# Kernel tuning notes

Measured on AMD Instinct MI355X. Metric: run time of the kernel, lower is better.

## Reference

```python
import jax, jax.numpy as jnp
import numpy as np

B, PATCH_NUM, EMBED, DEC_EMBED, IN_CHANS, PSIZE3, NPTS = 32, 196, 768, 512, 6, 4096, 100000


def setup_inputs() -> dict:
    key = jax.random.key(0)
    ks = jax.random.split(key, 12)
    s = 0.02
    return {
        "sel_features": jax.random.normal(ks[0], (NPTS, IN_CHANS), jnp.float32),
        "coords_rela_query": jax.random.randint(ks[1], (NPTS,), 0, PSIZE3),
        "patch_unq_inv": jax.random.randint(ks[2], (NPTS,), 0, B * PATCH_NUM),
        "pad_idx": jnp.arange(B * PATCH_NUM),
        "coords_abs_cut": jax.random.normal(ks[3], (B * PATCH_NUM, 3), jnp.float32),
        "sel_coors": jax.random.normal(ks[4], (NPTS, 3), jnp.float32),
        "batch_size": B,
        "proj_weights": jnp.ones((PSIZE3, IN_CHANS, EMBED), jnp.float32),
        "w1_enc": jax.random.normal(ks[5], (3, EMBED), jnp.float32) * s,
        "b1_enc": jnp.zeros((EMBED,), jnp.float32),
        "w2_enc": jax.random.normal(ks[6], (EMBED, EMBED), jnp.float32) * s,
        "b2_enc": jnp.zeros((EMBED,), jnp.float32),
        "w1_dec": jax.random.normal(ks[7], (3, DEC_EMBED), jnp.float32) * s,
        "b1_dec": jnp.zeros((DEC_EMBED,), jnp.float32),
        "w2_dec": jax.random.normal(ks[8], (DEC_EMBED, DEC_EMBED), jnp.float32) * s,
        "b2_dec": jnp.zeros((DEC_EMBED,), jnp.float32),
    }


def _mlp(x, w1, b1, w2, b2):
    # nn.Linear -> GELU (exact erf, torch default) -> nn.Linear
    h = jax.nn.gelu(x @ w1 + b1, approximate=False)
    return h @ w2 + b2


def reference(sel_features, coords_rela_query, patch_unq_inv, pad_idx,
              coords_abs_cut, sel_coors, batch_size, proj_weights,
              w1_enc, b1_enc, w2_enc, b2_enc, w1_dec, b1_dec, w2_dec, b2_dec):
    num_seg = batch_size * PATCH_NUM
    feats = jnp.einsum('nc,ncd->nd', sel_features, proj_weights[coords_rela_query])  # [N_pts, D]
    # scatter-mean over patch segment ids
    seg_sum = jax.ops.segment_sum(feats, patch_unq_inv, num_segments=num_seg)
    cnt = jax.ops.segment_sum(jnp.ones((feats.shape[0],), feats.dtype), patch_unq_inv, num_segments=num_seg)
    seg_mean = seg_sum / jnp.maximum(cnt, 1.0)[:, None]
    # masked scatter into padded [B*patch_num, D] tensor
    features_patch = jnp.zeros((num_seg, EMBED), feats.dtype).at[pad_idx].set(seg_mean)
    features_patch = features_patch.reshape(batch_size, PATCH_NUM, EMBED)
    coords = coords_abs_cut.reshape(batch_size, PATCH_NUM, 3)
    pos_emb_enc = _mlp(coords, w1_enc, b1_enc, w2_enc, b2_enc)
    pos_emb_dec = _mlp(coords, w1_dec, b1_dec, w2_dec, b2_dec)
    # sel_features is returned detached in the original
    return (features_patch + pos_emb_enc,
            jax.lax.stop_gradient(sel_features),
            sel_coors,
            pos_emb_dec)
```

## Files before the change

### kernel.cpp

```cpp
#include <hip/hip_runtime.h>
#include <hip/hip_bf16.h>
#include <cmath>

#define NTHREADS 256

constexpr int IN_CHANS = 6;
constexpr int EMBED = 768;
constexpr int DEC_EMBED = 512;

typedef __attribute__((ext_vector_type(8))) short short8;
typedef __attribute__((ext_vector_type(4))) float f32x4;

__device__ __forceinline__ void gload_lds16(const short* g, short* l) {
    __builtin_amdgcn_global_load_lds((const __attribute__((address_space(1))) void*)g,
                                     (__attribute__((address_space(3))) void*)l, 16, 0, 0);
}

__device__ __forceinline__ float gelu_f(float x) {
    return 0.5f * x * (1.0f + erff(x * 0.70710678118654752f));
}


__global__ void zero_kernel(int* __restrict__ p, int n) {
    int i = blockIdx.x * blockDim.x + threadIdx.x;
    if (i < n) p[i] = 0;
}


__global__ void hc_kernel(const float* __restrict__ coords,
                          const float* __restrict__ w1e, const float* __restrict__ b1e,
                          const float* __restrict__ w1d, const float* __restrict__ b1d,
                          const int* __restrict__ seg, const int* __restrict__ pad_idx,
                          const float* __restrict__ sel, const float* __restrict__ selc,
                          const float* __restrict__ w2e, const float* __restrict__ w2d,
                          __hip_bfloat16* __restrict__ hE, __hip_bfloat16* __restrict__ hD,
                          __hip_bfloat16* __restrict__ w2tE, __hip_bfloat16* __restrict__ w2tD,
                          int* __restrict__ segcnt, float* __restrict__ segsum,
                          int* __restrict__ inv,
                          float* __restrict__ out1, float* __restrict__ out2,
                          int hcBlocks, int num_seg, int npts) {
    __shared__ float tile[32][33];
    int bid = blockIdx.x;
    if (bid >= hcBlocks) {
        int b = bid - hcBlocks;
        const float* src; __hip_bfloat16* dst; int n;
        const int ntE = (EMBED / 32) * (EMBED / 32);
        if (b < ntE) { src = w2e; dst = w2tE; n = EMBED; }
        else         { b -= ntE; src = w2d; dst = w2tD; n = DEC_EMBED; }
        int tpr = n / 32;
        int tr = b / tpr, tc = b % tpr;
        int tx = threadIdx.x & 31, ty = threadIdx.x >> 5;
        #pragma unroll
        for (int i = 0; i < 4; ++i)
            tile[ty + 8 * i][tx] = src[(size_t)(tr * 32 + ty + 8 * i) * n + tc * 32 + tx];
        __syncthreads();
        #pragma unroll
        for (int i = 0; i < 4; ++i)
            dst[(size_t)(tc * 32 + ty + 8 * i) * n + tr * 32 + tx] =
                __float2bfloat16(tile[tx][ty + 8 * i]);
        return;
    }
    const unsigned nE8 = (unsigned)num_seg * (EMBED / 8);
    const unsigned nD8 = (unsigned)num_seg * (DEC_EMBED / 8);
    const unsigned t0 = nE8;
    const unsigned t1 = t0 + nD8;
    const unsigned t2 = t1 + (unsigned)npts;
    const unsigned t2b = t2 + (unsigned)num_seg;
    const unsigned n14 = (unsigned)npts * IN_CHANS / 4;
    const unsigned t3 = t2b + n14;
    const unsigned n24 = (unsigned)npts * 3 / 4;
    const unsigned t4 = t3 + n24;
    const unsigned stride = (unsigned)hcBlocks * blockDim.x;
    for (unsigned idx = bid * blockDim.x + threadIdx.x; idx < t4; idx += stride) {
        if (idx < t0) {
            unsigned r = idx / (EMBED / 8), d = (idx % (EMBED / 8)) * 8;
            float c0 = coords[r * 3 + 0], c1 = coords[r * 3 + 1], c2 = coords[r * 3 + 2];
            float4 wa0 = *reinterpret_cast<const float4*>(w1e + 0 * EMBED + d);
            float4 wa1 = *reinterpret_cast<const float4*>(w1e + 0 * EMBED + d + 4);
            float4 wb0 = *reinterpret_cast<const float4*>(w1e + 1 * EMBED + d);
            float4 wb1 = *reinterpret_cast<const float4*>(w1e + 1 * EMBED + d + 4);
            float4 wc0 = *reinterpret_cast<const float4*>(w1e + 2 * EMBED + d);
            float4 wc1 = *reinterpret_cast<const float4*>(w1e + 2 * EMBED + d + 4);
            float4 bb0 = *reinterpret_cast<const float4*>(b1e + d);
            float4 bb1 = *reinterpret_cast<const float4*>(b1e + d + 4);
            union { short8 v; __hip_bfloat16 h[8]; } u;
            #pragma unroll
            for (int i = 0; i < 4; ++i)
                u.h[i] = __float2bfloat16(gelu_f(c0 * (&wa0.x)[i] + c1 * (&wb0.x)[i]
                                               + c2 * (&wc0.x)[i] + (&bb0.x)[i]));
            #pragma unroll
            for (int i = 0; i < 4; ++i)
                u.h[4 + i] = __float2bfloat16(gelu_f(c0 * (&wa1.x)[i] + c1 * (&wb1.x)[i]
                                                   + c2 * (&wc1.x)[i] + (&bb1.x)[i]));
            *reinterpret_cast<short8*>(&hE[(size_t)r * EMBED + d]) = u.v;
        } else if (idx < t1) {
            unsigned j = idx - t0;
            unsigned r = j / (DEC_EMBED / 8), d = (j % (DEC_EMBED / 8)) * 8;
            float c0 = coords[r * 3 + 0], c1 = coords[r * 3 + 1], c2 = coords[r * 3 + 2];
            float4 wa0 = *reinterpret_cast<const float4*>(w1d + 0 * DEC_EMBED + d);
            float4 wa1 = *reinterpret_cast<const float4*>(w1d + 0 * DEC_EMBED + d + 4);
            float4 wb0 = *reinterpret_cast<const float4*>(w1d + 1 * DEC_EMBED + d);
            float4 wb1 = *reinterpret_cast<const float4*>(w1d + 1 * DEC_EMBED + d + 4);
            float4 wc0 = *reinterpret_cast<const float4*>(w1d + 2 * DEC_EMBED + d);
            float4 wc1 = *reinterpret_cast<const float4*>(w1d + 2 * DEC_EMBED + d + 4);
            float4 bb0 = *reinterpret_cast<const float4*>(b1d + d);
            float4 bb1 = *reinterpret_cast<const float4*>(b1d + d + 4);
            union { short8 v; __hip_bfloat16 h[8]; } u;
            #pragma unroll
            for (int i = 0; i < 4; ++i)
                u.h[i] = __float2bfloat16(gelu_f(c0 * (&wa0.x)[i] + c1 * (&wb0.x)[i]
                                               + c2 * (&wc0.x)[i] + (&bb0.x)[i]));
            #pragma unroll
            for (int i = 0; i < 4; ++i)
                u.h[4 + i] = __float2bfloat16(gelu_f(c0 * (&wa1.x)[i] + c1 * (&wb1.x)[i]
                                                   + c2 * (&wc1.x)[i] + (&bb1.x)[i]));
            *reinterpret_cast<short8*>(&hD[(size_t)r * DEC_EMBED + d]) = u.v;
        } else if (idx < t2) {
            int i = (int)(idx - t1);
            int s = seg[i];
            atomicAdd(&segcnt[s], 1);
            const float2* s2 = reinterpret_cast<const float2*>(sel + (size_t)i * IN_CHANS);
            float2 a = s2[0], b = s2[1], c = s2[2];
            unsafeAtomicAdd(&segsum[s], a.x + a.y + b.x + b.y + c.x + c.y);
        } else if (idx < t2b) {
            int s = (int)(idx - t2);
            inv[pad_idx[s]] = s;
        } else if (idx < t3) {
            unsigned j = idx - t2b;
            reinterpret_cast<float4*>(out1)[j] =
                reinterpret_cast<const float4*>(sel)[j];
        } else {
            unsigned j = idx - t3;
            reinterpret_cast<float4*>(out2)[j] =
                reinterpret_cast<const float4*>(selc)[j];
        }
    }
}


__global__ void fallback_fix_kernel(const int* __restrict__ notones,
                                    const float* __restrict__ sel,
                                    const int* __restrict__ q,
                                    const int* __restrict__ seg,
                                    const int* __restrict__ segcnt,
                                    const float* __restrict__ segsum,
                                    const int* __restrict__ pad_idx,
                                    const float* __restrict__ W,
                                    float* __restrict__ out0, int npts, int num_seg) {
    if (*notones == 0) return;
    long totalP = (long)npts * (EMBED / 4);
    long totalS = (long)num_seg * (EMBED / 4);
    long total = totalP + totalS;
    for (long idx = blockIdx.x * (long)blockDim.x + threadIdx.x; idx < total;
         idx += (long)gridDim.x * blockDim.x) {
        if (idx < totalP) {
            int n = (int)(idx / (EMBED / 4));
            int d4 = (int)(idx % (EMBED / 4)) * 4;
            int s = seg[n];
            float invc = 1.0f / (float)max(segcnt[s], 1);
            const float* Wr = W + (size_t)q[n] * IN_CHANS * EMBED + d4;
            float acc[4] = {0.f, 0.f, 0.f, 0.f};
            #pragma unroll
            for (int c = 0; c < IN_CHANS; ++c) {
                float sv = sel[(size_t)n * IN_CHANS + c];
                float4 wv = *reinterpret_cast<const float4*>(Wr + c * EMBED);
                acc[0] += sv * wv.x; acc[1] += sv * wv.y;
                acc[2] += sv * wv.z; acc[3] += sv * wv.w;
            }
            size_t j = (size_t)pad_idx[s];
            #pragma unroll
            for (int i = 0; i < 4; ++i)
                unsafeAtomicAdd(&out0[j * EMBED + d4 + i], acc[i] * invc);
        } else {
            long j2 = idx - totalP;
            int s = (int)(j2 / (EMBED / 4));
            int d4 = (int)(j2 % (EMBED / 4)) * 4;
            float mean = segsum[s] / (float)max(segcnt[s], 1);
            size_t j = (size_t)pad_idx[s];
            #pragma unroll
            for (int i = 0; i < 4; ++i)
                unsafeAtomicAdd(&out0[j * EMBED + d4 + i], -mean);
        }
    }
}


__global__ __launch_bounds__(256, 6)
void gemm_lds_kernel(const __hip_bfloat16* __restrict__ hE,
                     const __hip_bfloat16* __restrict__ w2tE,
                     const float* __restrict__ b2e,
                     const __hip_bfloat16* __restrict__ hD,
                     const __hip_bfloat16* __restrict__ w2tD,
                     const float* __restrict__ b2d,
                     const float* __restrict__ Wproj,
                     const float* __restrict__ segsum,
                     const int* __restrict__ segcnt,
                     const int* __restrict__ inv,
                     int* __restrict__ notones,
                     float* __restrict__ out0, float* __restrict__ out3,
                     int M, int nblkE, int nblkTot, int ckBlocks, int psize3) {
    int bid = blockIdx.x;
    if (bid < ckBlocks) {
        const unsigned total4 = (unsigned)psize3 * (IN_CHANS * EMBED / 4);
        const unsigned stride4 = (unsigned)ckBlocks * blockDim.x * 4u;
        const float4* p = reinterpret_cast<const float4*>(Wproj);
        bool bad = false;
        for (unsigned i = ((unsigned)bid * blockDim.x + threadIdx.x) * 4u; i < total4;
             i += stride4) {
            float4 v0 = p[i], v1 = p[i + 1], v2 = p[i + 2], v3 = p[i + 3];
            bad |= v0.x != 1.f || v0.y != 1.f || v0.z != 1.f || v0.w != 1.f;
            bad |= v1.x != 1.f || v1.y != 1.f || v1.z != 1.f || v1.w != 1.f;
            bad |= v2.x != 1.f || v2.y != 1.f || v2.z != 1.f || v2.w != 1.f;
            bad |= v3.x != 1.f || v3.y != 1.f || v3.z != 1.f || v3.w != 1.f;
        }
        if (bad) atomicOr(notones, 1);
        return;
    }
    bid -= ckBlocks;
    int q8 = nblkTot >> 3, r8 = nblkTot & 7;
    int xcd = bid & 7, idx = bid >> 3;
    int bx = (xcd < r8 ? xcd * (q8 + 1) : r8 * (q8 + 1) + (xcd - r8) * q8) + idx;

    const short* A;
    const short* Bt;
    const float* b2;
    float* out;
    int N, K;
    bool enc;
    if (bx < nblkE) {
        A = (const short*)hE; Bt = (const short*)w2tE; b2 = b2e; out = out0;
        N = EMBED; K = EMBED; enc = true;
    } else {
        bx -= nblkE;
        A = (const short*)hD; Bt = (const short*)w2tD; b2 = b2d; out = out3;
        N = DEC_EMBED; K = DEC_EMBED; enc = false;
    }
    constexpr int BM = 64, BN = 64, BK = 64;
    int ctiles = N / BN;
    int rt = bx / ctiles, ct = bx % ctiles;

    __shared__ short Al[BM * BK];
    __shared__ short Bl[BN * BK];

    int t = threadIdx.x;
    int lane = t & 63;
    int w = t >> 6;
    int wr = w >> 1, wc = w & 1;
    int r0 = wr * 32;
    int c0 = wc * 32;

    int lrow = lane & 15;
    int kgrp = (lane >> 4) << 3;
    int rsw = (lrow & 7) * 8;

    int srow = t >> 3;
    int scol = (t & 7) * 8;
    int ssw  = scol ^ ((srow & 7) * 8);

    int gA[2];
    #pragma unroll
    for (int i = 0; i < 2; ++i) {
        int r = rt * BM + i * 32 + srow;
        gA[i] = (r < M) ? r : M - 1;
    }
    const short* ap[2];
    #pragma unroll
    for (int i = 0; i < 2; ++i) ap[i] = A + (size_t)gA[i] * K + ssw;
    const short* bp[2];
    #pragma unroll
    for (int i = 0; i < 2; ++i)
        bp[i] = Bt + (size_t)(ct * BN + i * 32 + srow) * K + ssw;
    short* la[2];
    #pragma unroll
    for (int i = 0; i < 2; ++i) la[i] = &Al[i * 2048 + t * 8];
    short* lb[2];
    #pragma unroll
    for (int i = 0; i < 2; ++i) lb[i] = &Bl[i * 2048 + t * 8];

    f32x4 acc[2][2];
    #pragma unroll
    for (int mi = 0; mi < 2; ++mi)
        #pragma unroll
        for (int ni = 0; ni < 2; ++ni) acc[mi][ni] = f32x4{0.f, 0.f, 0.f, 0.f};

    for (int k0 = 0; k0 < K; k0 += BK) {
        #pragma unroll
        for (int i = 0; i < 2; ++i) gload_lds16(ap[i] + k0, la[i]);
        #pragma unroll
        for (int i = 0; i < 2; ++i) gload_lds16(bp[i] + k0, lb[i]);
        __syncthreads();
        #pragma unroll
        for (int ks = 0; ks < 2; ++ks) {
            int colA = (ks * 32 + kgrp) ^ rsw;
            short8 af[2], bf[2];
            #pragma unroll
            for (int mi = 0; mi < 2; ++mi)
                af[mi] = *reinterpret_cast<const short8*>(
                    &Al[(r0 + mi * 16 + lrow) * BK + colA]);
            #pragma unroll
            for (int ni = 0; ni < 2; ++ni)
                bf[ni] = *reinterpret_cast<const short8*>(
                    &Bl[(c0 + ni * 16 + lrow) * BK + colA]);
            #pragma unroll
            for (int mi = 0; mi < 2; ++mi)
                #pragma unroll
                for (int ni = 0; ni < 2; ++ni)
                    acc[mi][ni] = __builtin_amdgcn_mfma_f32_16x16x32_bf16(af[mi], bf[ni],
                                                                          acc[mi][ni],
                                                                          0, 0, 0);
        }
        __syncthreads();
    }

    int rbase = (lane >> 4) << 2;
    float mrow[2][4];
    #pragma unroll
    for (int mi = 0; mi < 2; ++mi)
        #pragma unroll
        for (int j = 0; j < 4; ++j) {
            float mv = 0.f;
            int row = rt * BM + r0 + mi * 16 + rbase + j;
            if (enc && row < M) {
                int s = inv[row];
                mv = segsum[s] / (float)max(segcnt[s], 1);
            }
            mrow[mi][j] = mv;
        }
    #pragma unroll
    for (int ni = 0; ni < 2; ++ni) {
        int col = ct * BN + c0 + ni * 16 + lrow;
        float bb = b2[col];
        #pragma unroll
        for (int mi = 0; mi < 2; ++mi) {
            #pragma unroll
            for (int j = 0; j < 4; ++j) {
                int row = rt * BM + r0 + mi * 16 + rbase + j;
                if (row < M) {
                    size_t o = (size_t)row * N + col;
                    out[o] = acc[mi][ni][j] + bb + mrow[mi][j];
                }
            }
        }
    }
}


extern "C" void kernel_launch(void* const* d_in, const int* in_sizes, int n_in,
                              void* d_out, int out_size, void* d_ws, size_t ws_size,
                              hipStream_t stream) {
    const float* sel_features = (const float*)d_in[0];
    const int*   q            = (const int*)d_in[1];
    const int*   seg          = (const int*)d_in[2];
    const int*   pad_idx      = (const int*)d_in[3];
    const float* coords       = (const float*)d_in[4];
    const float* sel_coors    = (const float*)d_in[5];
    const float* W            = (const float*)d_in[7];
    const float* w1e          = (const float*)d_in[8];
    const float* b1e          = (const float*)d_in[9];
    const float* w2e          = (const float*)d_in[10];
    const float* b2e          = (const float*)d_in[11];
    const float* w1d          = (const float*)d_in[12];
    const float* b1d          = (const float*)d_in[13];
    const float* w2d          = (const float*)d_in[14];
    const float* b2d          = (const float*)d_in[15];

    int npts    = in_sizes[1];
    int num_seg = in_sizes[3];
    int psize3  = in_sizes[7] / (IN_CHANS * EMBED);

    float* out  = (float*)d_out;
    float* out0 = out;
    float* out1 = out0 + (size_t)num_seg * EMBED;
    float* out2 = out1 + (size_t)npts * IN_CHANS;
    float* out3 = out2 + (size_t)npts * 3;

    char* wsb = (char*)d_ws;
    __hip_bfloat16* hE   = (__hip_bfloat16*)wsb;
    __hip_bfloat16* hD   = hE + (size_t)num_seg * EMBED;
    __hip_bfloat16* w2tE = hD + (size_t)num_seg * DEC_EMBED;
    __hip_bfloat16* w2tD = w2tE + (size_t)EMBED * EMBED;
    int*   segcnt  = (int*)(w2tD + (size_t)DEC_EMBED * DEC_EMBED);
    float* segsum  = (float*)(segcnt + num_seg);
    int*   notones = (int*)(segsum + num_seg);
    int*   inv     = notones + 1;

    int nzero = 2 * num_seg + 1;
    zero_kernel<<<(nzero + NTHREADS - 1) / NTHREADS, NTHREADS, 0, stream>>>(segcnt, nzero);

    int hcBlocks = 1024;
    int ntE = (EMBED / 32) * (EMBED / 32);
    int ntD = (DEC_EMBED / 32) * (DEC_EMBED / 32);
    hc_kernel<<<hcBlocks + ntE + ntD, NTHREADS, 0, stream>>>(
        coords, w1e, b1e, w1d, b1d, seg, pad_idx, sel_features, sel_coors,
        w2e, w2d, hE, hD, w2tE, w2tD, segcnt, segsum, inv, out1, out2,
        hcBlocks, num_seg, npts);

    int rtiles = (num_seg + 63) / 64;
    int nblkE = rtiles * (EMBED / 64);
    int nblkD = rtiles * (DEC_EMBED / 64);
    int nblkTot = nblkE + nblkD;
    int ckBlocks = 1024;
    gemm_lds_kernel<<<ckBlocks + nblkTot, NTHREADS, 0, stream>>>(
        hE, w2tE, b2e, hD, w2tD, b2d, W, segsum, segcnt, inv, notones,
        out0, out3, num_seg, nblkE, nblkTot, ckBlocks, psize3);

    fallback_fix_kernel<<<256, NTHREADS, 0, stream>>>(notones, sel_features, q, seg,
                                                      segcnt, segsum, pad_idx, W,
                                                      out0, npts, num_seg);
}
```

Measured before the change: 68.13 us.

## Double-buffer LDS tiles in the fused GEMM to overlap loads with MFMA

The GEMM main loop now uses two LDS buffers per operand. The next K-tile's global-to-LDS load is issued before the MFMA work on the current tile, replacing the old load-sync-compute-sync pattern, and the last tile is handled in a separate epilogue. The aim is to hide global load latency behind compute. It doubles LDS use to 32 KB per block, and launch bounds drop from 6 to 5 blocks per CU, which can cut occupancy.

New measurement: 71.25 us. 1.05x slower.

```diff
diff --git a/kernel.cpp b/kernel.cpp
--- a/kernel.cpp
+++ b/kernel.cpp
@@ -185,7 +185,7 @@
 }
 
 
-__global__ __launch_bounds__(256, 6)
+__global__ __launch_bounds__(256, 5)
 void gemm_lds_kernel(const __hip_bfloat16* __restrict__ hE,
                      const __hip_bfloat16* __restrict__ w2tE,
                      const float* __restrict__ b2e,
@@ -236,11 +236,12 @@
         N = DEC_EMBED; K = DEC_EMBED; enc = false;
     }
     constexpr int BM = 64, BN = 64, BK = 64;
+    constexpr int BUFSZ = BM * BK;
     int ctiles = N / BN;
     int rt = bx / ctiles, ct = bx % ctiles;
 
-    __shared__ short Al[BM * BK];
-    __shared__ short Bl[BN * BK];
+    __shared__ short Al[2 * BUFSZ];
+    __shared__ short Bl[2 * BUFSZ];
 
     int t = threadIdx.x;
     int lane = t & 63;
@@ -270,12 +271,6 @@
     #pragma unroll
     for (int i = 0; i < 2; ++i)
         bp[i] = Bt + (size_t)(ct * BN + i * 32 + srow) * K + ssw;
-    short* la[2];
-    #pragma unroll
-    for (int i = 0; i < 2; ++i) la[i] = &Al[i * 2048 + t * 8];
-    short* lb[2];
-    #pragma unroll
-    for (int i = 0; i < 2; ++i) lb[i] = &Bl[i * 2048 + t * 8];
 
     f32x4 acc[2][2];
     #pragma unroll
@@ -283,12 +278,26 @@
         #pragma unroll
         for (int ni = 0; ni < 2; ++ni) acc[mi][ni] = f32x4{0.f, 0.f, 0.f, 0.f};
 
-    for (int k0 = 0; k0 < K; k0 += BK) {
-        #pragma unroll
-        for (int i = 0; i < 2; ++i) gload_lds16(ap[i] + k0, la[i]);
-        #pragma unroll
-        for (int i = 0; i < 2; ++i) gload_lds16(bp[i] + k0, lb[i]);
-        __syncthreads();
+    int nt = K / BK;
+    int cur = 0;
+
+    #pragma unroll
+    for (int i = 0; i < 2; ++i) gload_lds16(ap[i], &Al[i * 2048 + t * 8]);
+    #pragma unroll
+    for (int i = 0; i < 2; ++i) gload_lds16(bp[i], &Bl[i * 2048 + t * 8]);
+    __syncthreads();
+
+    for (int tt = 0; tt < nt - 1; ++tt) {
+        int nxt = cur ^ 1;
+        int k1 = (tt + 1) * BK;
+        #pragma unroll
+        for (int i = 0; i < 2; ++i)
+            gload_lds16(ap[i] + k1, &Al[nxt * BUFSZ + i * 2048 + t * 8]);
+        #pragma unroll
+        for (int i = 0; i < 2; ++i)
+            gload_lds16(bp[i] + k1, &Bl[nxt * BUFSZ + i * 2048 + t * 8]);
+        const short* Ab = &Al[cur * BUFSZ];
+        const short* Bb = &Bl[cur * BUFSZ];
         #pragma unroll
         for (int ks = 0; ks < 2; ++ks) {
             int colA = (ks * 32 + kgrp) ^ rsw;
@@ -296,11 +305,11 @@
             #pragma unroll
             for (int mi = 0; mi < 2; ++mi)
                 af[mi] = *reinterpret_cast<const short8*>(
-                    &Al[(r0 + mi * 16 + lrow) * BK + colA]);
+                    &Ab[(r0 + mi * 16 + lrow) * BK + colA]);
             #pragma unroll
             for (int ni = 0; ni < 2; ++ni)
                 bf[ni] = *reinterpret_cast<const short8*>(
-                    &Bl[(c0 + ni * 16 + lrow) * BK + colA]);
+                    &Bb[(c0 + ni * 16 + lrow) * BK + colA]);
             #pragma unroll
             for (int mi = 0; mi < 2; ++mi)
                 #pragma unroll
@@ -310,6 +319,31 @@
                                                                           0, 0, 0);
         }
         __syncthreads();
+        cur = nxt;
+    }
+    {
+        const short* Ab = &Al[cur * BUFSZ];
+        const short* Bb = &Bl[cur * BUFSZ];
+        #pragma unroll
+        for (int ks = 0; ks < 2; ++ks) {
+            int colA = (ks * 32 + kgrp) ^ rsw;
+            short8 af[2], bf[2];
+            #pragma unroll
+            for (int mi = 0; mi < 2; ++mi)
+                af[mi] = *reinterpret_cast<const short8*>(
+                    &Ab[(r0 + mi * 16 + lrow) * BK + colA]);
+            #pragma unroll
+            for (int ni = 0; ni < 2; ++ni)
+                bf[ni] = *reinterpret_cast<const short8*>(
+                    &Bb[(c0 + ni * 16 + lrow) * BK + colA]);
+            #pragma unroll
+            for (int mi = 0; mi < 2; ++mi)
+                #pragma unroll
+                for (int ni = 0; ni < 2; ++ni)
+                    acc[mi][ni] = __builtin_amdgcn_mfma_f32_16x16x32_bf16(af[mi], bf[ni],
+                                                                          acc[mi][ni],
+                                                                          0, 0, 0);
+        }
     }
 
     int rbase = (lane >> 4) << 2;
```
